# Kernel optimization log

Measured on AMD Instinct MI355X. Metric: run time of the kernel, lower is better.

The kernel has to match this reference:

```python
import jax, jax.numpy as jnp
import numpy as np

N_NODES = 50000
N_EDGES = 800000
IN_CH = 128
HEADS = 4
OUT_CH = 32
NEG_SLOPE = 0.2


def setup_inputs() -> dict:
    key = jax.random.key(0)
    ks = jax.random.split(key, 7)
    x = jax.random.normal(ks[0], (N_NODES, IN_CH), dtype=jnp.float32)
    src = jax.random.randint(ks[1], (N_EDGES,), 0, N_NODES, dtype=jnp.int32)
    dst = jax.random.randint(ks[2], (N_EDGES,), 0, N_NODES, dtype=jnp.int32)
    W = jax.random.normal(ks[3], (IN_CH, HEADS * OUT_CH), dtype=jnp.float32) * (1.0 / np.sqrt(IN_CH))
    attn_l = jax.random.normal(ks[4], (HEADS, OUT_CH), dtype=jnp.float32) * 0.1
    attn_r = jax.random.normal(ks[5], (HEADS, OUT_CH), dtype=jnp.float32) * 0.1
    bias = jnp.zeros((HEADS * OUT_CH,), dtype=jnp.float32)
    return {"x": x, "src": src, "dst": dst, "W": W, "attn_l": attn_l, "attn_r": attn_r, "bias": bias}


def reference(x, src, dst, W, attn_l, attn_r, bias):
    n = x.shape[0]
    # Linear projection -> per-head features [N, H, D]
    feat = (x @ W).reshape(n, HEADS, OUT_CH)
    # Node-level attention terms [N, H]
    el = jnp.einsum('nhd,hd->nh', feat, attn_l)
    er = jnp.einsum('nhd,hd->nh', feat, attn_r)
    # Edge attention logits [E, H]
    e = jax.nn.leaky_relu(el[src] + er[dst], negative_slope=NEG_SLOPE)
    # Segment softmax over incoming edges of each dst node
    m = jax.ops.segment_max(e, dst, num_segments=n)          # [N, H]
    m = jnp.where(jnp.isfinite(m), m, 0.0)
    ex = jnp.exp(e - m[dst])                                  # [E, H]
    s = jax.ops.segment_sum(ex, dst, num_segments=n)          # [N, H]
    alpha = ex / s[dst]                                       # [E, H]
    # Weighted message aggregation: scatter-add to dst [N, H, D]
    msg = feat[src] * alpha[:, :, None]
    out = jax.ops.segment_sum(msg, dst, num_segments=n)
    out = out + bias.reshape(HEADS, OUT_CH)
    # agg='mean' over heads -> [N, D]
    return out.mean(axis=1)
```

## Files before the change

### kernel.cpp

```cpp
#include <hip/hip_runtime.h>

#define IN_CH 128
#define NEG_SLOPE 0.2f

typedef short bf16x8 __attribute__((ext_vector_type(8)));
typedef float floatx4 __attribute__((ext_vector_type(4)));

static __device__ __forceinline__ unsigned short f2bf(float f) {
    union { float f; unsigned int u; } a; a.f = f;
    unsigned int u = a.u;
    u += 0x7fffu + ((u >> 16) & 1u);
    return (unsigned short)(u >> 16);
}

__global__ void k_rank(const int* __restrict__ dst, int* __restrict__ cnt,
                       int* __restrict__ rank, int E,
                       const float* __restrict__ W, unsigned short* __restrict__ Wtb) {
    int e = blockIdx.x * 256 + threadIdx.x;
    if (blockIdx.x < 64) {
        int i = blockIdx.x * 256 + threadIdx.x;
        int n = i >> 7, k = i & 127;
        Wtb[i] = f2bf(W[(size_t)k * 128 + n]);
    }
    if (e < E) rank[e] = atomicAdd(&cnt[dst[e]], 1);
}

__global__ __launch_bounds__(256) void k_partsum(const int* __restrict__ cnt,
                                                 int* __restrict__ blocksum, int N) {
    int base = blockIdx.x * 1024 + threadIdx.x * 4;
    int s = 0;
    if (base + 3 < N) {
        int4 v = *(const int4*)(cnt + base);
        s = v.x + v.y + v.z + v.w;
    } else {
        for (int i = 0; i < 4; ++i)
            if (base + i < N) s += cnt[base + i];
    }
#pragma unroll
    for (int off = 32; off; off >>= 1) s += __shfl_down(s, off);
    __shared__ int red[4];
    if ((threadIdx.x & 63) == 0) red[threadIdx.x >> 6] = s;
    __syncthreads();
    if (threadIdx.x == 0) blocksum[blockIdx.x] = red[0] + red[1] + red[2] + red[3];
}

__global__ __launch_bounds__(256) void k_scanwrite(const int* __restrict__ cnt,
                                                   const int* __restrict__ blocksum,
                                                   int* __restrict__ rowstart, int N, int NB) {
    __shared__ int boff[65];
    if (threadIdx.x < 64) {
        int t = threadIdx.x;
        int v = (t < NB) ? blocksum[t] : 0;
#pragma unroll
        for (int off = 1; off < 64; off <<= 1) {
            int u = __shfl_up(v, off);
            if (t >= off) v += u;
        }
        boff[t + 1] = v;
        if (t == 0) boff[0] = 0;
    }
    __syncthreads();
    int base = blockIdx.x * 1024 + threadIdx.x * 4;
    int v[4];
    int s = 0;
#pragma unroll
    for (int i = 0; i < 4; ++i) {
        v[i] = (base + i < N) ? cnt[base + i] : 0;
        s += v[i];
    }
    int lane = threadIdx.x & 63, wid = threadIdx.x >> 6;
    int inc = s;
#pragma unroll
    for (int off = 1; off < 64; off <<= 1) {
        int u = __shfl_up(inc, off);
        if (lane >= off) inc += u;
    }
    __shared__ int wsum[4];
    if (lane == 63) wsum[wid] = inc;
    __syncthreads();
    int woff = 0;
    for (int i = 0; i < wid; ++i) woff += wsum[i];
    int run = boff[blockIdx.x] + woff + (inc - s);
#pragma unroll
    for (int i = 0; i < 4; ++i) {
        int id = base + i;
        if (id < N) {
            rowstart[id] = run;
            run += v[i];
        }
    }
    if (blockIdx.x == 0 && threadIdx.x == 0) rowstart[N] = boff[NB];
}

__global__ void k_place(const int* __restrict__ src, const int* __restrict__ dst,
                        const int* __restrict__ rank, const int* __restrict__ rowstart,
                        int* __restrict__ esrc, int E) {
    int e = blockIdx.x * 256 + threadIdx.x;
    if (e >= E) return;
    esrc[rowstart[dst[e]] + rank[e]] = src[e];
}

__global__ __launch_bounds__(256) void k_gemm(const float* __restrict__ x,
                                              const unsigned short* __restrict__ Wtb,
                                              const float* __restrict__ attn_l,
                                              const float* __restrict__ attn_r,
                                              unsigned short* __restrict__ featb,
                                              float* __restrict__ el,
                                              float* __restrict__ er, int N) {
    __shared__ __align__(16) unsigned short Al[16 * 136];
    __shared__ float elpart[2][8][16];
    int m0 = blockIdx.x * 16;
    const float4* xt = (const float4*)(x + (size_t)m0 * 128);
#pragma unroll
    for (int i = 0; i < 2; ++i) {
        int f4i = threadIdx.x + 256 * i;
        float4 u = xt[f4i];
        int f = f4i * 4;
        int row = f >> 7, col = f & 127;
        ushort4 pk;
        pk.x = f2bf(u.x); pk.y = f2bf(u.y); pk.z = f2bf(u.z); pk.w = f2bf(u.w);
        *(ushort4*)(Al + row * 136 + col) = pk;
    }
    __syncthreads();
    int wave = threadIdx.x >> 6;
    int lane = threadIdx.x & 63;
    int l15 = lane & 15;
    int quad = lane >> 4;
    int n0 = wave * 16;
    int n1 = wave * 16 + 64;
    const unsigned short* ap = Al + l15 * 136 + quad * 8;
    const unsigned short* bp0 = Wtb + (size_t)(n0 + l15) * 128 + quad * 8;
    const unsigned short* bp1 = Wtb + (size_t)(n1 + l15) * 128 + quad * 8;
    floatx4 acc0 = {0.f, 0.f, 0.f, 0.f};
    floatx4 acc1 = {0.f, 0.f, 0.f, 0.f};
#pragma unroll
    for (int kk = 0; kk < 4; ++kk) {
        bf16x8 a  = *(const bf16x8*)(ap + kk * 32);
        bf16x8 b0 = *(const bf16x8*)(bp0 + kk * 32);
        bf16x8 b1 = *(const bf16x8*)(bp1 + kk * 32);
        acc0 = __builtin_amdgcn_mfma_f32_16x16x32_bf16(a, b0, acc0, 0, 0, 0);
        acc1 = __builtin_amdgcn_mfma_f32_16x16x32_bf16(a, b1, acc1, 0, 0, 0);
    }
    float al0 = attn_l[n0 + l15], al1 = attn_l[n1 + l15];
    float ar0 = attn_r[n0 + l15], ar1 = attn_r[n1 + l15];
    float pl0[4], pl1[4], pr0[4], pr1[4];
#pragma unroll
    for (int r = 0; r < 4; ++r) {
        pl0[r] = acc0[r] * al0; pl1[r] = acc1[r] * al1;
        pr0[r] = acc0[r] * ar0; pr1[r] = acc1[r] * ar1;
#pragma unroll
        for (int m = 1; m <= 8; m <<= 1) {
            pl0[r] += __shfl_xor(pl0[r], m);
            pl1[r] += __shfl_xor(pl1[r], m);
            pr0[r] += __shfl_xor(pr0[r], m);
            pr1[r] += __shfl_xor(pr1[r], m);
        }
    }
    if (l15 == 0) {
#pragma unroll
        for (int r = 0; r < 4; ++r) {
            int row = quad * 4 + r;
            elpart[0][wave][row]     = pl0[r];
            elpart[0][wave + 4][row] = pl1[r];
            elpart[1][wave][row]     = pr0[r];
            elpart[1][wave + 4][row] = pr1[r];
        }
    }
#pragma unroll
    for (int r = 0; r < 4; ++r) {
        size_t row = (size_t)(m0 + quad * 4 + r) * 128;
        featb[row + n0 + l15] = f2bf(acc0[r]);
        featb[row + n1 + l15] = f2bf(acc1[r]);
    }
    __syncthreads();
    if (threadIdx.x < 128) {
        int lr = threadIdx.x >> 6;
        int t = threadIdx.x & 63;
        int row = t & 15, h = t >> 4;
        float v = elpart[lr][2 * h][row] + elpart[lr][2 * h + 1][row];
        float* dp = lr ? er : el;
        dp[(size_t)(m0 + row) * 4 + h] = v;
    }
}

__global__ __launch_bounds__(256) void k_node(const int* __restrict__ rowstart,
                                              const int* __restrict__ esrc,
                                              const float* __restrict__ el,
                                              const float* __restrict__ er,
                                              const unsigned short* __restrict__ featb,
                                              const float* __restrict__ bias,
                                              float* __restrict__ out, int N) {
    int n = blockIdx.x * 4 + (threadIdx.x >> 6);
    if (n >= N) return;
    int lane = threadIdx.x & 63;
    int g = lane >> 4;
    int r = lane & 15;
    int h = r >> 2;
    int row0 = rowstart[n], row1 = rowstart[n + 1];
    float erh = er[(size_t)n * 4 + h];
    float s = 0.f;
    float a0 = 0.f, a1 = 0.f, a2 = 0.f, a3 = 0.f;
    float a4 = 0.f, a5 = 0.f, a6 = 0.f, a7 = 0.f;
#pragma unroll 2
    for (int j = row0 + g; j < row1; j += 4) {
        int sn = esrc[j];
        float t = el[(size_t)sn * 4 + h] + erh;
        float e = __expf(t > 0.f ? t : NEG_SLOPE * t);
        s += e;
        uint4 q = *(const uint4*)(featb + (size_t)sn * 128 + r * 8);
        a0 += e * __uint_as_float(q.x << 16);
        a1 += e * __uint_as_float(q.x & 0xffff0000u);
        a2 += e * __uint_as_float(q.y << 16);
        a3 += e * __uint_as_float(q.y & 0xffff0000u);
        a4 += e * __uint_as_float(q.z << 16);
        a5 += e * __uint_as_float(q.z & 0xffff0000u);
        a6 += e * __uint_as_float(q.w << 16);
        a7 += e * __uint_as_float(q.w & 0xffff0000u);
    }
    s  += __shfl_xor(s, 16);  s  += __shfl_xor(s, 32);
    a0 += __shfl_xor(a0, 16); a0 += __shfl_xor(a0, 32);
    a1 += __shfl_xor(a1, 16); a1 += __shfl_xor(a1, 32);
    a2 += __shfl_xor(a2, 16); a2 += __shfl_xor(a2, 32);
    a3 += __shfl_xor(a3, 16); a3 += __shfl_xor(a3, 32);
    a4 += __shfl_xor(a4, 16); a4 += __shfl_xor(a4, 32);
    a5 += __shfl_xor(a5, 16); a5 += __shfl_xor(a5, 32);
    a6 += __shfl_xor(a6, 16); a6 += __shfl_xor(a6, 32);
    a7 += __shfl_xor(a7, 16); a7 += __shfl_xor(a7, 32);
    float inv = (row1 > row0) ? 0.25f / s : 0.f;
    a0 *= inv; a1 *= inv; a2 *= inv; a3 *= inv;
    a4 *= inv; a5 *= inv; a6 *= inv; a7 *= inv;
    a0 += __shfl_xor(a0, 4); a0 += __shfl_xor(a0, 8);
    a1 += __shfl_xor(a1, 4); a1 += __shfl_xor(a1, 8);
    a2 += __shfl_xor(a2, 4); a2 += __shfl_xor(a2, 8);
    a3 += __shfl_xor(a3, 4); a3 += __shfl_xor(a3, 8);
    a4 += __shfl_xor(a4, 4); a4 += __shfl_xor(a4, 8);
    a5 += __shfl_xor(a5, 4); a5 += __shfl_xor(a5, 8);
    a6 += __shfl_xor(a6, 4); a6 += __shfl_xor(a6, 8);
    a7 += __shfl_xor(a7, 4); a7 += __shfl_xor(a7, 8);
    if (lane < 4) {
        int dd = lane * 8;
        float4 o0, o1;
        o0.x = a0 + 0.25f * (bias[dd + 0] + bias[32 + dd + 0] + bias[64 + dd + 0] + bias[96 + dd + 0]);
        o0.y = a1 + 0.25f * (bias[dd + 1] + bias[32 + dd + 1] + bias[64 + dd + 1] + bias[96 + dd + 1]);
        o0.z = a2 + 0.25f * (bias[dd + 2] + bias[32 + dd + 2] + bias[64 + dd + 2] + bias[96 + dd + 2]);
        o0.w = a3 + 0.25f * (bias[dd + 3] + bias[32 + dd + 3] + bias[64 + dd + 3] + bias[96 + dd + 3]);
        o1.x = a4 + 0.25f * (bias[dd + 4] + bias[32 + dd + 4] + bias[64 + dd + 4] + bias[96 + dd + 4]);
        o1.y = a5 + 0.25f * (bias[dd + 5] + bias[32 + dd + 5] + bias[64 + dd + 5] + bias[96 + dd + 5]);
        o1.z = a6 + 0.25f * (bias[dd + 6] + bias[32 + dd + 6] + bias[64 + dd + 6] + bias[96 + dd + 6]);
        o1.w = a7 + 0.25f * (bias[dd + 7] + bias[32 + dd + 7] + bias[64 + dd + 7] + bias[96 + dd + 7]);
        *(float4*)(out + (size_t)n * 32 + dd) = o0;
        *(float4*)(out + (size_t)n * 32 + dd + 4) = o1;
    }
}

extern "C" void kernel_launch(void* const* d_in, const int* in_sizes, int n_in,
                              void* d_out, int out_size, void* d_ws, size_t ws_size,
                              hipStream_t stream) {
    const float* x      = (const float*)d_in[0];
    const int*   src    = (const int*)d_in[1];
    const int*   dst    = (const int*)d_in[2];
    const float* W      = (const float*)d_in[3];
    const float* attn_l = (const float*)d_in[4];
    const float* attn_r = (const float*)d_in[5];
    const float* bias   = (const float*)d_in[6];
    float* out = (float*)d_out;

    int N = in_sizes[0] / IN_CH;
    int E = in_sizes[1];
    int NB = (N + 1023) / 1024;

    char* w = (char*)d_ws;
    unsigned short* featb = (unsigned short*)w; w += (size_t)N * 128 * 2;
    unsigned short* Wtb   = (unsigned short*)w; w += 128 * 128 * 2;
    float* el       = (float*)w;  w += (size_t)N * 4 * 4;
    float* er       = (float*)w;  w += (size_t)N * 4 * 4;
    int*   cnt      = (int*)w;    w += (size_t)N * 4;
    int*   rank     = (int*)w;    w += (size_t)E * 4;
    int*   rowstart = (int*)w;    w += (size_t)(N + 1) * 4;
    int*   esrc     = (int*)w;    w += (size_t)E * 4;
    int*   blocksum = (int*)w;    w += 64 * 4;

    hipMemsetAsync(cnt, 0, (size_t)N * 4, stream);
    k_rank<<<(E + 255) / 256, 256, 0, stream>>>(dst, cnt, rank, E, W, Wtb);
    k_partsum<<<NB, 256, 0, stream>>>(cnt, blocksum, N);
    k_scanwrite<<<NB, 256, 0, stream>>>(cnt, blocksum, rowstart, N, NB);
    k_gemm<<<N / 16, 256, 0, stream>>>(x, Wtb, attn_l, attn_r, featb, el, er, N);
    k_place<<<(E + 255) / 256, 256, 0, stream>>>(src, dst, rank, rowstart, esrc, E);
    k_node<<<(N + 3) / 4, 256, 0, stream>>>(rowstart, esrc, el, er, featb, bias, out, N);
}
```

Before: 188.1 us.

## Fuse GEMM with edge ranking, replace memset with prep kernel, prefetch esrc

Merges the projection GEMM and the atomic edge-rank pass into one launch that splits its blocks by role, so both run concurrently. The cnt memset becomes part of a prep kernel that also converts W to bf16. The node kernel now software-prefetches the next source index so the gather address is ready sooner. This cuts launch count and inter-kernel gaps. The cost is more register pressure in the node loop and mixed block types competing for the same CUs.

```diff
diff --git a/kernel.cpp b/kernel.cpp
--- a/kernel.cpp
+++ b/kernel.cpp
@@ -13,102 +13,33 @@
     return (unsigned short)(u >> 16);
 }
 
-__global__ void k_rank(const int* __restrict__ dst, int* __restrict__ cnt,
-                       int* __restrict__ rank, int E,
-                       const float* __restrict__ W, unsigned short* __restrict__ Wtb) {
-    int e = blockIdx.x * 256 + threadIdx.x;
-    if (blockIdx.x < 64) {
-        int i = blockIdx.x * 256 + threadIdx.x;
+__global__ void k_prep(const float* __restrict__ W, unsigned short* __restrict__ Wtb,
+                       int* __restrict__ cnt, int N) {
+    int i = blockIdx.x * 256 + threadIdx.x;
+    if (i < N) cnt[i] = 0;
+    if (i < 128 * 128) {
         int n = i >> 7, k = i & 127;
         Wtb[i] = f2bf(W[(size_t)k * 128 + n]);
     }
-    if (e < E) rank[e] = atomicAdd(&cnt[dst[e]], 1);
-}
-
-__global__ __launch_bounds__(256) void k_partsum(const int* __restrict__ cnt,
-                                                 int* __restrict__ blocksum, int N) {
-    int base = blockIdx.x * 1024 + threadIdx.x * 4;
-    int s = 0;
-    if (base + 3 < N) {
-        int4 v = *(const int4*)(cnt + base);
-        s = v.x + v.y + v.z + v.w;
-    } else {
-        for (int i = 0; i < 4; ++i)
-            if (base + i < N) s += cnt[base + i];
-    }
-#pragma unroll
-    for (int off = 32; off; off >>= 1) s += __shfl_down(s, off);
-    __shared__ int red[4];
-    if ((threadIdx.x & 63) == 0) red[threadIdx.x >> 6] = s;
-    __syncthreads();
-    if (threadIdx.x == 0) blocksum[blockIdx.x] = red[0] + red[1] + red[2] + red[3];
-}
-
-__global__ __launch_bounds__(256) void k_scanwrite(const int* __restrict__ cnt,
-                                                   const int* __restrict__ blocksum,
-                                                   int* __restrict__ rowstart, int N, int NB) {
-    __shared__ int boff[65];
-    if (threadIdx.x < 64) {
-        int t = threadIdx.x;
-        int v = (t < NB) ? blocksum[t] : 0;
-#pragma unroll
-        for (int off = 1; off < 64; off <<= 1) {
-            int u = __shfl_up(v, off);
-            if (t >= off) v += u;
-        }
-        boff[t + 1] = v;
-        if (t == 0) boff[0] = 0;
-    }
-    __syncthreads();
-    int base = blockIdx.x * 1024 + threadIdx.x * 4;
-    int v[4];
-    int s = 0;
-#pragma unroll
-    for (int i = 0; i < 4; ++i) {
-        v[i] = (base + i < N) ? cnt[base + i] : 0;
-        s += v[i];
-    }
-    int lane = threadIdx.x & 63, wid = threadIdx.x >> 6;
-    int inc = s;
-#pragma unroll
-    for (int off = 1; off < 64; off <<= 1) {
-        int u = __shfl_up(inc, off);
-        if (lane >= off) inc += u;
-    }
-    __shared__ int wsum[4];
-    if (lane == 63) wsum[wid] = inc;
-    __syncthreads();
-    int woff = 0;
-    for (int i = 0; i < wid; ++i) woff += wsum[i];
-    int run = boff[blockIdx.x] + woff + (inc - s);
-#pragma unroll
-    for (int i = 0; i < 4; ++i) {
-        int id = base + i;
-        if (id < N) {
-            rowstart[id] = run;
-            run += v[i];
-        }
-    }
-    if (blockIdx.x == 0 && threadIdx.x == 0) rowstart[N] = boff[NB];
-}
-
-__global__ void k_place(const int* __restrict__ src, const int* __restrict__ dst,
-                        const int* __restrict__ rank, const int* __restrict__ rowstart,
-                        int* __restrict__ esrc, int E) {
-    int e = blockIdx.x * 256 + threadIdx.x;
-    if (e >= E) return;
-    esrc[rowstart[dst[e]] + rank[e]] = src[e];
-}
-
-__global__ __launch_bounds__(256) void k_gemm(const float* __restrict__ x,
-                                              const unsigned short* __restrict__ Wtb,
-                                              const float* __restrict__ attn_l,
-                                              const float* __restrict__ attn_r,
-                                              unsigned short* __restrict__ featb,
-                                              float* __restrict__ el,
-                                              float* __restrict__ er, int N) {
+}
+
+__global__ __launch_bounds__(256) void k_gemmrank(const float* __restrict__ x,
+                                                  const unsigned short* __restrict__ Wtb,
+                                                  const float* __restrict__ attn_l,
+                                                  const float* __restrict__ attn_r,
+                                                  unsigned short* __restrict__ featb,
+                                                  float* __restrict__ el,
+                                                  float* __restrict__ er, int N,
+                                                  const int* __restrict__ dst,
+                                                  int* __restrict__ cnt,
+                                                  int* __restrict__ rank, int E, int GB) {
     __shared__ __align__(16) unsigned short Al[16 * 136];
     __shared__ float elpart[2][8][16];
+    if ((int)blockIdx.x >= GB) {
+        int e = (blockIdx.x - GB) * 256 + threadIdx.x;
+        if (e < E) rank[e] = atomicAdd(&cnt[dst[e]], 1);
+        return;
+    }
     int m0 = blockIdx.x * 16;
     const float4* xt = (const float4*)(x + (size_t)m0 * 128);
 #pragma unroll
@@ -181,6 +112,81 @@
         float* dp = lr ? er : el;
         dp[(size_t)(m0 + row) * 4 + h] = v;
     }
+}
+
+__global__ __launch_bounds__(256) void k_partsum(const int* __restrict__ cnt,
+                                                 int* __restrict__ blocksum, int N) {
+    int base = blockIdx.x * 1024 + threadIdx.x * 4;
+    int s = 0;
+    if (base + 3 < N) {
+        int4 v = *(const int4*)(cnt + base);
+        s = v.x + v.y + v.z + v.w;
+    } else {
+        for (int i = 0; i < 4; ++i)
+            if (base + i < N) s += cnt[base + i];
+    }
+#pragma unroll
+    for (int off = 32; off; off >>= 1) s += __shfl_down(s, off);
+    __shared__ int red[4];
+    if ((threadIdx.x & 63) == 0) red[threadIdx.x >> 6] = s;
+    __syncthreads();
+    if (threadIdx.x == 0) blocksum[blockIdx.x] = red[0] + red[1] + red[2] + red[3];
+}
+
+__global__ __launch_bounds__(256) void k_scanwrite(const int* __restrict__ cnt,
+                                                   const int* __restrict__ blocksum,
+                                                   int* __restrict__ rowstart, int N, int NB) {
+    __shared__ int boff[65];
+    if (threadIdx.x < 64) {
+        int t = threadIdx.x;
+        int v = (t < NB) ? blocksum[t] : 0;
+#pragma unroll
+        for (int off = 1; off < 64; off <<= 1) {
+            int u = __shfl_up(v, off);
+            if (t >= off) v += u;
+        }
+        boff[t + 1] = v;
+        if (t == 0) boff[0] = 0;
+    }
+    __syncthreads();
+    int base = blockIdx.x * 1024 + threadIdx.x * 4;
+    int v[4];
+    int s = 0;
+#pragma unroll
+    for (int i = 0; i < 4; ++i) {
+        v[i] = (base + i < N) ? cnt[base + i] : 0;
+        s += v[i];
+    }
+    int lane = threadIdx.x & 63, wid = threadIdx.x >> 6;
+    int inc = s;
+#pragma unroll
+    for (int off = 1; off < 64; off <<= 1) {
+        int u = __shfl_up(inc, off);
+        if (lane >= off) inc += u;
+    }
+    __shared__ int wsum[4];
+    if (lane == 63) wsum[wid] = inc;
+    __syncthreads();
+    int woff = 0;
+    for (int i = 0; i < wid; ++i) woff += wsum[i];
+    int run = boff[blockIdx.x] + woff + (inc - s);
+#pragma unroll
+    for (int i = 0; i < 4; ++i) {
+        int id = base + i;
+        if (id < N) {
+            rowstart[id] = run;
+            run += v[i];
+        }
+    }
+    if (blockIdx.x == 0 && threadIdx.x == 0) rowstart[N] = boff[NB];
+}
+
+__global__ void k_place(const int* __restrict__ src, const int* __restrict__ dst,
+                        const int* __restrict__ rank, const int* __restrict__ rowstart,
+                        int* __restrict__ esrc, int E) {
+    int e = blockIdx.x * 256 + threadIdx.x;
+    if (e >= E) return;
+    esrc[rowstart[dst[e]] + rank[e]] = src[e];
 }
 
 __global__ __launch_bounds__(256) void k_node(const int* __restrict__ rowstart,
@@ -201,9 +207,11 @@
     float s = 0.f;
     float a0 = 0.f, a1 = 0.f, a2 = 0.f, a3 = 0.f;
     float a4 = 0.f, a5 = 0.f, a6 = 0.f, a7 = 0.f;
+    int j = row0 + g;
+    int sn = (j < row1) ? esrc[j] : 0;
 #pragma unroll 2
-    for (int j = row0 + g; j < row1; j += 4) {
-        int sn = esrc[j];
+    for (; j < row1; j += 4) {
+        int snn = (j + 4 < row1) ? esrc[j + 4] : 0;
         float t = el[(size_t)sn * 4 + h] + erh;
         float e = __expf(t > 0.f ? t : NEG_SLOPE * t);
         s += e;
@@ -216,6 +224,7 @@
         a5 += e * __uint_as_float(q.z & 0xffff0000u);
         a6 += e * __uint_as_float(q.w << 16);
         a7 += e * __uint_as_float(q.w & 0xffff0000u);
+        sn = snn;
     }
     s  += __shfl_xor(s, 16);  s  += __shfl_xor(s, 32);
     a0 += __shfl_xor(a0, 16); a0 += __shfl_xor(a0, 32);
@@ -268,6 +277,8 @@
     int N = in_sizes[0] / IN_CH;
     int E = in_sizes[1];
     int NB = (N + 1023) / 1024;
+    int GB = N / 16;
+    int RB = (E + 255) / 256;
 
     char* w = (char*)d_ws;
     unsigned short* featb = (unsigned short*)w; w += (size_t)N * 128 * 2;
@@ -280,11 +291,11 @@
     int*   esrc     = (int*)w;    w += (size_t)E * 4;
     int*   blocksum = (int*)w;    w += 64 * 4;
 
-    hipMemsetAsync(cnt, 0, (size_t)N * 4, stream);
-    k_rank<<<(E + 255) / 256, 256, 0, stream>>>(dst, cnt, rank, E, W, Wtb);
+    k_prep<<<(N + 255) / 256, 256, 0, stream>>>(W, Wtb, cnt, N);
+    k_gemmrank<<<GB + RB, 256, 0, stream>>>(x, Wtb, attn_l, attn_r, featb, el, er, N,
+                                            dst, cnt, rank, E, GB);
     k_partsum<<<NB, 256, 0, stream>>>(cnt, blocksum, N);
     k_scanwrite<<<NB, 256, 0, stream>>>(cnt, blocksum, rowstart, N, NB);
-    k_gemm<<<N / 16, 256, 0, stream>>>(x, Wtb, attn_l, attn_r, featb, el, er, N);
     k_place<<<(E + 255) / 256, 256, 0, stream>>>(src, dst, rank, rowstart, esrc, E);
     k_node<<<(N + 3) / 4, 256, 0, stream>>>(rowstart, esrc, el, er, featb, bias, out, N);
 }
```

Result: faster. 182.7 us (-2.9%).
